# Kernel optimization log

Hardware: AMD Instinct MI355X
Metric: run time of the kernel (lower is better)

Reference implementation:

```python
import jax, jax.numpy as jnp
import numpy as np

N_NODES = 100000
N_EDGES = 1600000


def setup_inputs() -> dict:
    key = jax.random.key(0)
    ks = jax.random.split(key, 16)
    d_emb, d_mlp, d_lstm = 128, 256, 256
    B, C, T = 8, 4, 128
    return {
        "input_ids": jax.random.randint(ks[0], (B, C, T), 0, N_NODES, dtype=jnp.int64 if jax.config.jax_enable_x64 else jnp.int32),
        "input_mask": jnp.ones((B, C, T), dtype=jnp.int32),
        "labels": jax.random.uniform(ks[1], (B, C), dtype=jnp.float32),
        "src": jax.random.randint(ks[2], (N_EDGES,), 0, N_NODES),
        "dst": jax.random.randint(ks[3], (N_EDGES,), 0, N_NODES),
        "edge_value": jax.random.uniform(ks[4], (N_EDGES,), dtype=jnp.float32),
        "node_emb": jax.random.normal(ks[5], (N_NODES, d_emb), dtype=jnp.float32),
        "W1": jax.random.normal(ks[6], (d_mlp, d_emb), dtype=jnp.float32) * 0.05,
        "b1": jax.random.normal(ks[7], (d_mlp,), dtype=jnp.float32) * 0.05,
        "w_ih": jax.random.normal(ks[8], (4 * d_lstm, d_mlp), dtype=jnp.float32) * 0.05,
        "w_hh": jax.random.normal(ks[9], (4 * d_lstm, d_lstm), dtype=jnp.float32) * 0.05,
        "b_ih": jax.random.normal(ks[10], (4 * d_lstm,), dtype=jnp.float32) * 0.05,
        "b_hh": jax.random.normal(ks[11], (4 * d_lstm,), dtype=jnp.float32) * 0.05,
        "W2": jax.random.normal(ks[12], (1, d_lstm), dtype=jnp.float32) * 0.05,
        "b2": jax.random.normal(ks[13], (1,), dtype=jnp.float32) * 0.05,
    }


def reference(input_ids, input_mask, labels, src, dst, edge_value,
              node_emb, W1, b1, w_ih, w_hh, b_ih, b_hh, W2, b2):
    N = node_emb.shape[0]
    # edge-weighted mean message passing: u_mul_e('embedding','value') -> mean
    m = node_emb[src] * edge_value[:, None]                       # [E, d_emb]
    agg = jax.ops.segment_sum(m, dst, num_segments=N)             # [N, d_emb]
    cnt = jax.ops.segment_sum(jnp.ones_like(edge_value), dst, num_segments=N)
    h_nodes = agg / jnp.maximum(cnt, 1.0)[:, None]
    # linear1 on all nodes
    t_nodes = h_nodes @ W1.T + b1                                  # [N, d_mlp]
    B, C, T = input_ids.shape
    x = t_nodes[input_ids.reshape(B * C, T)]                       # [BC, T, d_mlp]
    lengths = input_mask.sum(axis=-1).reshape(B * C)               # [BC]
    H = w_hh.shape[1]

    def step(carry, xt):
        h, c = carry
        gates = xt @ w_ih.T + b_ih + h @ w_hh.T + b_hh
        i, f, g, o = jnp.split(gates, 4, axis=-1)  # torch LSTM gate order
        c = jax.nn.sigmoid(f) * c + jax.nn.sigmoid(i) * jnp.tanh(g)
        h = jax.nn.sigmoid(o) * jnp.tanh(c)
        return (h, c), h

    h0 = jnp.zeros((B * C, H), x.dtype)
    _, hs = jax.lax.scan(step, (h0, h0), jnp.swapaxes(x, 0, 1))    # [T, BC, H]
    hs = jnp.swapaxes(hs, 0, 1)                                    # [BC, T, H]
    idx = (lengths - 1).astype(jnp.int32)[:, None, None]
    h_last = jnp.take_along_axis(hs, jnp.broadcast_to(idx, (B * C, 1, H)), axis=1)[:, 0, :]
    scores = (h_last @ W2.T + b2).reshape(B, C)                    # [B, 4]
    p = jax.nn.softmax(scores, axis=1)
    # BCEWithLogits applied to softmaxed scores (as in the original)
    error = jnp.mean(jnp.maximum(p, 0) - p * labels + jnp.log1p(jnp.exp(-jnp.abs(p))))
    predictions = jnp.argmax(p, axis=1)
    return error, predictions
```

## Files before the change

### kernel.cpp

```cpp
#include <hip/hip_runtime.h>
#include <math.h>

#define NNODES 100000
#define NEDGES 1600000
#define NPOS   4096
#define NSEQ   32
#define TSTEPS 128

typedef float f32x4 __attribute__((ext_vector_type(4)));
typedef unsigned u32x4 __attribute__((ext_vector_type(4)));
typedef _Float16 h2v __attribute__((ext_vector_type(2)));

#define OFF_SLOT   0
#define OFF_AGG    400128
#define OFF_CNT    2497280
#define OFF_WF     2513664
#define OFF_BIASF  3037952
#define OFF_PREG   3042048
#define OFF_HS     19819264
#define OFF_WR  OFF_AGG
#define OFF_WL  (OFF_AGG + 98304)
#define OFF_WS  (OFF_AGG + 245760)

static __device__ __forceinline__ float fdot2(unsigned w, unsigned h, float acc) {
#if __has_builtin(__builtin_amdgcn_fdot2)
  h2v wv, hv;
  __builtin_memcpy(&wv, &w, 4);
  __builtin_memcpy(&hv, &h, 4);
  return __builtin_amdgcn_fdot2(wv, hv, acc, false);
#else
  asm("v_dot2_f32_f16 %0, %1, %2, %0" : "+v"(acc) : "v"(w), "v"(h));
  return acc;
#endif
}

static __device__ __forceinline__ float dotq(u32x4 w, u32x4 h, float a) {
  a = fdot2(w[0], h[0], a);
  a = fdot2(w[1], h[1], a);
  a = fdot2(w[2], h[2], a);
  a = fdot2(w[3], h[3], a);
  return a;
}

__global__ void k_init(int* slotmap, float* agg, float* cnt, float* hs0) {
  int i = blockIdx.x * blockDim.x + threadIdx.x;
  int stride = gridDim.x * blockDim.x;
  for (int idx = i; idx < 4096 * 128; idx += stride) agg[idx] = 0.f;
  for (int idx = i; idx < NNODES; idx += stride) slotmap[idx] = -1;
  for (int idx = i; idx < 4096; idx += stride) cnt[idx] = 0.f;
  for (int idx = i; idx < 8192; idx += stride) hs0[idx] = 0.f;
}

__global__ void k_mark(const int* __restrict__ input_ids, int* __restrict__ slotmap) {
  int p = blockIdx.x * blockDim.x + threadIdx.x;
  if (p < NPOS) atomicCAS(&slotmap[input_ids[p]], -1, p);
}

__global__ void k_edge(const int* __restrict__ src, const int* __restrict__ dst,
                       const float* __restrict__ ev, const float* __restrict__ emb,
                       const int* __restrict__ slotmap,
                       float* __restrict__ agg, float* __restrict__ cnt) {
  int e = blockIdx.x * 256 + threadIdx.x;
  int lane = threadIdx.x & 63;
  int d = dst[e];
  int slot = slotmap[d];
  int sn = 0; float vv = 0.f;
  if (slot >= 0) { sn = src[e]; vv = ev[e]; }
  unsigned long long m = __ballot(slot >= 0);
  while (m) {
    int j = __ffsll(m) - 1;
    m &= m - 1;
    int sl = __shfl(slot, j);
    int s2 = __shfl(sn, j);
    float v = __shfl(vv, j);
    float2 em = *(const float2*)&emb[(size_t)s2 * 128 + 2 * lane];
    atomicAdd(&agg[sl * 128 + 2 * lane],     em.x * v);
    atomicAdd(&agg[sl * 128 + 2 * lane + 1], em.y * v);
    if (lane == 0) atomicAdd(&cnt[sl], 1.f);
  }
}

__global__ void k_div(float* __restrict__ agg, const float* __restrict__ cnt) {
  int i = blockIdx.x * blockDim.x + threadIdx.x;
  agg[i] /= fmaxf(cnt[i >> 7], 1.f);
}

__global__ void k_fuse(const float* __restrict__ w_ih, const float* __restrict__ W1,
                       const float* __restrict__ b1, const float* __restrict__ b_ih,
                       const float* __restrict__ b_hh,
                       float* __restrict__ Wf, float* __restrict__ bf) {
  int row = blockIdx.x;
  int e = threadIdx.x;
  float acc = 0.f;
  for (int m2 = 0; m2 < 256; ++m2) acc += w_ih[row * 256 + m2] * W1[m2 * 128 + e];
  Wf[row * 128 + e] = acc;
  if (e == 0) {
    float bacc = b_ih[row] + b_hh[row];
    for (int m2 = 0; m2 < 256; ++m2) bacc += w_ih[row * 256 + m2] * b1[m2];
    bf[row] = bacc;
  }
}

__global__ __launch_bounds__(256, 2) void k_pregemm(
    const float* __restrict__ hnode, const float* __restrict__ Wf,
    const float* __restrict__ bf, const int* __restrict__ slotmap,
    const int* __restrict__ input_ids, float* __restrict__ preg) {
  __shared__ float Ash[64][132];
  __shared__ float Bsh[64][132];
  __shared__ int slots[64];
  int tid = threadIdx.x;
  int bm = (blockIdx.x & 63) * 64;
  int bn = (blockIdx.x >> 6) * 64;
  if (tid < 64) slots[tid] = slotmap[input_ids[bm + tid]];
  __syncthreads();
#pragma unroll
  for (int i = 0; i < 8; ++i) {
    int idx = tid + 256 * i;
    int r = idx >> 5, c = idx & 31;
    *(float4*)&Ash[r][c * 4] = *(const float4*)&hnode[slots[r] * 128 + c * 4];
    *(float4*)&Bsh[r][c * 4] = *(const float4*)&Wf[(bn + r) * 128 + c * 4];
  }
  __syncthreads();
  int tx = tid & 15, ty = tid >> 4;
  float acc[4][4] = {};
  for (int k = 0; k < 128; k += 4) {
    float4 a[4], bb[4];
#pragma unroll
    for (int i = 0; i < 4; ++i) a[i] = *(const float4*)&Ash[tx + 16 * i][k];
#pragma unroll
    for (int j = 0; j < 4; ++j) bb[j] = *(const float4*)&Bsh[ty + 16 * j][k];
#pragma unroll
    for (int i = 0; i < 4; ++i)
#pragma unroll
      for (int j = 0; j < 4; ++j)
        acc[i][j] += a[i].x * bb[j].x + a[i].y * bb[j].y + a[i].z * bb[j].z + a[i].w * bb[j].w;
  }
#pragma unroll
  for (int j = 0; j < 4; ++j) {
    int row = bn + ty + 16 * j;
    float bias = bf[row];
    int q  = row >> 8;
    int mm = (row >> 5) & 7;
    int dl = row & 31;
#pragma unroll
    for (int i = 0; i < 4; ++i) {
      int p = bm + tx + 16 * i;
      int s = p >> 7, tt = p & 127;
      preg[(((size_t)(tt * 32 + s) * 8 + mm) * 4 + q) * 32 + dl] = acc[i][j] + bias;
    }
  }
}

__global__ void k_wcvt(const float* __restrict__ w_hh, unsigned* __restrict__ wR,
                       unsigned* __restrict__ wL, unsigned* __restrict__ wS) {
  int idx = blockIdx.x * 256 + threadIdx.x;
  int row = idx >> 7;
  int j   = idx & 127;
  float x0 = w_hh[(size_t)row * 256 + 2 * j];
  float x1 = w_hh[(size_t)row * 256 + 2 * j + 1];
  union { _Float16 f[2]; unsigned u; } pk;
  pk.f[0] = (_Float16)x0;
  pk.f[1] = (_Float16)x1;
  int q = row >> 8, dd = row & 255;
  int kseg = j >> 5, p = j & 31;
  int c = p >> 2, l = p & 3;
  int tid = kseg * 256 + dd;
  if (q == 0 && c < 6) {
    wR[(c * 4 + l) * 1024 + tid] = pk.u;
  } else if (q == 0) {
    wL[((c - 6) * 1024 + tid) * 4 + l] = pk.u;
  } else if (q == 1 && c < 7) {
    wL[((2 + c) * 1024 + tid) * 4 + l] = pk.u;
  } else if (q == 1) {
    wS[(14 * 1024 + tid) * 4 + l] = pk.u;
  } else if (q == 2) {
    wS[(((c < 7) ? (2 * c) : 15) * 1024 + tid) * 4 + l] = pk.u;
  } else {
    wS[(((c < 7) ? (2 * c + 1) : 16) * 1024 + tid) * 4 + l] = pk.u;
  }
}

__global__ __launch_bounds__(1024) void k_lstm(
    const unsigned* __restrict__ wR, const unsigned* __restrict__ wL,
    const unsigned* __restrict__ wS, const float* __restrict__ preg,
    float* __restrict__ hs) {
  __shared__ __align__(16) unsigned whL[9 * 1024 * 4];
  __shared__ __align__(16) unsigned h16[128];
  __shared__ __align__(16) float    accb[3 * 256 * 4];
  const int tid  = threadIdx.x;
  const int s    = blockIdx.x;
  const int kseg = tid >> 8;
  const int d    = tid & 255;
  const bool owner = (kseg == 0);

  u32x4 rq[6];
#pragma unroll
  for (int qr = 0; qr < 6; ++qr)
#pragma unroll
    for (int l = 0; l < 4; ++l)
      rq[qr][l] = wR[(qr * 4 + l) * 1024 + tid];
  {
    const u32x4* src = (const u32x4*)wL;
    u32x4* dst = (u32x4*)whL;
#pragma unroll
    for (int lc = 0; lc < 9; ++lc)
      dst[lc * 1024 + tid] = src[lc * 1024 + tid];
  }
  if (tid < 128) h16[tid] = 0u;
  float c_st = 0.f;
  __syncthreads();

  const u32x4* hqp = (const u32x4*)h16 + kseg * 8;
  const u32x4* lq  = (const u32x4*)whL + tid;
  const u32x4* sq  = (const u32x4*)wS + tid;

  for (int t = 0; t < TSTEPS; ++t) {
    float pg[4] = {0.f, 0.f, 0.f, 0.f};
    if (owner) {
      const float* pb = preg + (((size_t)(t * 32 + s) * 8 + (d >> 5)) * 4) * 32
                        + (d & 31);
#pragma unroll
      for (int q = 0; q < 4; ++q) pg[q] = pb[q * 32];
    }
    float a0 = 0.f, a1 = 0.f, a2 = 0.f, a3 = 0.f;
#pragma unroll
    for (int c = 0; c < 8; ++c) {
      u32x4 h4 = hqp[c];
      u32x4 w0 = (c < 6) ? rq[c] : lq[(c - 6) * 1024];
      u32x4 w1 = (c < 7) ? lq[(2 + c) * 1024] : sq[14 * 1024];
      u32x4 w2 = sq[((c < 7) ? (2 * c) : 15) * 1024];
      u32x4 w3 = sq[((c < 7) ? (2 * c + 1) : 16) * 1024];
      a0 = dotq(w0, h4, a0);
      a1 = dotq(w1, h4, a1);
      a2 = dotq(w2, h4, a2);
      a3 = dotq(w3, h4, a3);
    }
    if (!owner) {
      f32x4 r; r.x = a0; r.y = a1; r.z = a2; r.w = a3;
      *(f32x4*)&accb[((kseg - 1) * 256 + d) * 4] = r;
    }
    __syncthreads();
    if (owner) {
      f32x4 r0 = *(const f32x4*)&accb[(0 * 256 + d) * 4];
      f32x4 r1 = *(const f32x4*)&accb[(1 * 256 + d) * 4];
      f32x4 r2 = *(const f32x4*)&accb[(2 * 256 + d) * 4];
      float gi = a0 + r0.x + r1.x + r2.x + pg[0];
      float gf = a1 + r0.y + r1.y + r2.y + pg[1];
      float gg = a2 + r0.z + r1.z + r2.z + pg[2];
      float go = a3 + r0.w + r1.w + r2.w + pg[3];
      float si = 1.f / (1.f + expf(-gi));
      float sf = 1.f / (1.f + expf(-gf));
      float so = 1.f / (1.f + expf(-go));
      float cc = sf * c_st + si * tanhf(gg);
      float hh = so * tanhf(cc);
      c_st = cc;
      ((_Float16*)h16)[d] = (_Float16)hh;
      hs[(size_t)(t + 1) * 8192 + s * 256 + d] = hh;
    }
    __syncthreads();
  }
}

__global__ void k_final(const float* __restrict__ hs, const int* __restrict__ mask,
                        const float* __restrict__ labels, const float* __restrict__ W2,
                        const float* __restrict__ b2, float* __restrict__ out) {
  __shared__ float scores[32];
  __shared__ float errpart[8];
  int tid = threadIdx.x;
  if (tid < 32) {
    int len = 0;
    for (int t = 0; t < 128; ++t) len += mask[tid * 128 + t];
    if (len < 1) len = 1;
    const float* hl = hs + (size_t)len * 8192 + tid * 256;
    float acc = b2[0];
    for (int k = 0; k < 256; ++k) acc += hl[k] * W2[k];
    scores[tid] = acc;
  }
  __syncthreads();
  if (tid < 8) {
    float sc[4];
#pragma unroll
    for (int i = 0; i < 4; ++i) sc[i] = scores[tid * 4 + i];
    float mx = fmaxf(fmaxf(sc[0], sc[1]), fmaxf(sc[2], sc[3]));
    float ex[4], ssum = 0.f;
#pragma unroll
    for (int i = 0; i < 4; ++i) { ex[i] = expf(sc[i] - mx); ssum += ex[i]; }
    float esum = 0.f; int am = 0; float best = -1e30f;
#pragma unroll
    for (int i = 0; i < 4; ++i) {
      float p = ex[i] / ssum;
      float li = labels[tid * 4 + i];
      esum += fmaxf(p, 0.f) - p * li + log1pf(expf(-fabsf(p)));
      if (p > best) { best = p; am = i; }
    }
    errpart[tid] = esum;
    out[1 + tid] = (float)am;
  }
  __syncthreads();
  if (tid == 0) {
    float e = 0.f;
    for (int i = 0; i < 8; ++i) e += errpart[i];
    out[0] = e / 32.f;
  }
}

extern "C" void kernel_launch(void* const* d_in, const int* in_sizes, int n_in,
                              void* d_out, int out_size, void* d_ws, size_t ws_size,
                              hipStream_t stream) {
  const int*   input_ids  = (const int*)d_in[0];
  const int*   input_mask = (const int*)d_in[1];
  const float* labels     = (const float*)d_in[2];
  const int*   src        = (const int*)d_in[3];
  const int*   dst        = (const int*)d_in[4];
  const float* ev         = (const float*)d_in[5];
  const float* node_emb   = (const float*)d_in[6];
  const float* W1         = (const float*)d_in[7];
  const float* b1         = (const float*)d_in[8];
  const float* w_ih       = (const float*)d_in[9];
  const float* w_hh       = (const float*)d_in[10];
  const float* b_ih       = (const float*)d_in[11];
  const float* b_hh       = (const float*)d_in[12];
  const float* W2         = (const float*)d_in[13];
  const float* b2         = (const float*)d_in[14];
  float* out = (float*)d_out;
  char* ws = (char*)d_ws;
  int*      slotmap = (int*)(ws + OFF_SLOT);
  float*    agg     = (float*)(ws + OFF_AGG);
  float*    cnt     = (float*)(ws + OFF_CNT);
  float*    Wf      = (float*)(ws + OFF_WF);
  float*    biasf   = (float*)(ws + OFF_BIASF);
  float*    preg    = (float*)(ws + OFF_PREG);
  float*    hs      = (float*)(ws + OFF_HS);
  unsigned* wRimg   = (unsigned*)(ws + OFF_WR);
  unsigned* wLimg   = (unsigned*)(ws + OFF_WL);
  unsigned* wSimg   = (unsigned*)(ws + OFF_WS);

  hipLaunchKernelGGL(k_init,    dim3(2048), dim3(256),  0, stream, slotmap, agg, cnt, hs);
  hipLaunchKernelGGL(k_mark,    dim3(16),   dim3(256),  0, stream, input_ids, slotmap);
  hipLaunchKernelGGL(k_edge,    dim3(6250), dim3(256),  0, stream, src, dst, ev, node_emb, slotmap, agg, cnt);
  hipLaunchKernelGGL(k_div,     dim3(2048), dim3(256),  0, stream, agg, cnt);
  hipLaunchKernelGGL(k_fuse,    dim3(1024), dim3(128),  0, stream, w_ih, W1, b1, b_ih, b_hh, Wf, biasf);
  hipLaunchKernelGGL(k_pregemm, dim3(1024), dim3(256),  0, stream, agg, Wf, biasf, slotmap, input_ids, preg);
  hipLaunchKernelGGL(k_wcvt,    dim3(512),  dim3(256),  0, stream, w_hh, wRimg, wLimg, wSimg);
  hipLaunchKernelGGL(k_lstm,    dim3(NSEQ), dim3(1024), 0, stream, wRimg, wLimg, wSimg, preg, hs);
  hipLaunchKernelGGL(k_final,   dim3(1),    dim3(64),   0, stream, hs, input_mask, labels, W2, b2, out);
}
```

Before: 334.0 us.

## Replace atomic edge scatter with counting-sort bucketing and per-slot accumulation

Edges whose destination is a referenced slot are counted, prefix-summed and bucketed into a compact per-slot edge list. One wave per slot then accumulates the weighted embeddings in registers and writes them once. This removes the float atomics on the aggregation buffer and the need to zero it. The cost is two extra passes over the edge arrays plus a single-block prefix-scan launch, and scatter order is nondeterministic, so float summation order can vary between runs.

```diff
diff --git a/kernel.cpp b/kernel.cpp
--- a/kernel.cpp
+++ b/kernel.cpp
@@ -42,12 +42,11 @@
   return a;
 }
 
-__global__ void k_init(int* slotmap, float* agg, float* cnt, float* hs0) {
+__global__ void k_init(int* slotmap, int* icnt, float* hs0) {
   int i = blockIdx.x * blockDim.x + threadIdx.x;
   int stride = gridDim.x * blockDim.x;
-  for (int idx = i; idx < 4096 * 128; idx += stride) agg[idx] = 0.f;
   for (int idx = i; idx < NNODES; idx += stride) slotmap[idx] = -1;
-  for (int idx = i; idx < 4096; idx += stride) cnt[idx] = 0.f;
+  for (int idx = i; idx < 4096; idx += stride) icnt[idx] = 0;
   for (int idx = i; idx < 8192; idx += stride) hs0[idx] = 0.f;
 }
 
@@ -56,33 +55,76 @@
   if (p < NPOS) atomicCAS(&slotmap[input_ids[p]], -1, p);
 }
 
-__global__ void k_edge(const int* __restrict__ src, const int* __restrict__ dst,
-                       const float* __restrict__ ev, const float* __restrict__ emb,
-                       const int* __restrict__ slotmap,
-                       float* __restrict__ agg, float* __restrict__ cnt) {
+__global__ void k_cnt(const int* __restrict__ dst, const int* __restrict__ slotmap,
+                      int* __restrict__ icnt) {
   int e = blockIdx.x * 256 + threadIdx.x;
+  int slot = slotmap[dst[e]];
+  if (slot >= 0) atomicAdd(&icnt[slot], 1);
+}
+
+__global__ void k_prefix(const int* __restrict__ icnt, int* __restrict__ offs,
+                         int* __restrict__ curs) {
+  __shared__ int part[256];
+  int tid = threadIdx.x;
+  int base = tid * 16;
+  int local[16];
+  int s = 0;
+  for (int i = 0; i < 16; ++i) { local[i] = s; s += icnt[base + i]; }
+  part[tid] = s;
+  __syncthreads();
+  for (int off = 1; off < 256; off <<= 1) {
+    int v = part[tid];
+    int add = (tid >= off) ? part[tid - off] : 0;
+    __syncthreads();
+    part[tid] = v + add;
+    __syncthreads();
+  }
+  int excl = (tid == 0) ? 0 : part[tid - 1];
+  for (int i = 0; i < 16; ++i) {
+    int o = excl + local[i];
+    offs[base + i] = o;
+    curs[base + i] = o;
+  }
+}
+
+__global__ void k_scat(const int* __restrict__ dst, const int* __restrict__ slotmap,
+                       const int* __restrict__ src, const float* __restrict__ ev,
+                       int* __restrict__ curs, int2* __restrict__ ebuf) {
+  int e = blockIdx.x * 256 + threadIdx.x;
+  int slot = slotmap[dst[e]];
+  if (slot >= 0) {
+    int idx = atomicAdd(&curs[slot], 1);
+    int2 r;
+    r.x = src[e];
+    r.y = __float_as_int(ev[e]);
+    ebuf[idx] = r;
+  }
+}
+
+__global__ void k_acc(const int2* __restrict__ ebuf, const int* __restrict__ offs,
+                      const int* __restrict__ icnt, const float* __restrict__ emb,
+                      float* __restrict__ agg) {
+  int wave = threadIdx.x >> 6;
   int lane = threadIdx.x & 63;
-  int d = dst[e];
-  int slot = slotmap[d];
-  int sn = 0; float vv = 0.f;
-  if (slot >= 0) { sn = src[e]; vv = ev[e]; }
-  unsigned long long m = __ballot(slot >= 0);
-  while (m) {
-    int j = __ffsll(m) - 1;
-    m &= m - 1;
-    int sl = __shfl(slot, j);
-    int s2 = __shfl(sn, j);
-    float v = __shfl(vv, j);
-    float2 em = *(const float2*)&emb[(size_t)s2 * 128 + 2 * lane];
-    atomicAdd(&agg[sl * 128 + 2 * lane],     em.x * v);
-    atomicAdd(&agg[sl * 128 + 2 * lane + 1], em.y * v);
-    if (lane == 0) atomicAdd(&cnt[sl], 1.f);
-  }
-}
-
-__global__ void k_div(float* __restrict__ agg, const float* __restrict__ cnt) {
+  int slot = blockIdx.x * 4 + wave;
+  int base = offs[slot], n = icnt[slot];
+  float a0 = 0.f, a1 = 0.f;
+  for (int i = 0; i < n; ++i) {
+    int2 r = ebuf[base + i];
+    float2 em = *(const float2*)&emb[(size_t)r.x * 128 + 2 * lane];
+    float v = __int_as_float(r.y);
+    a0 += em.x * v;
+    a1 += em.y * v;
+  }
+  float2 o;
+  o.x = a0;
+  o.y = a1;
+  *(float2*)&agg[slot * 128 + 2 * lane] = o;
+}
+
+__global__ void k_div(float* __restrict__ agg, const int* __restrict__ icnt) {
   int i = blockIdx.x * blockDim.x + threadIdx.x;
-  agg[i] /= fmaxf(cnt[i >> 7], 1.f);
+  agg[i] /= fmaxf((float)icnt[i >> 7], 1.f);
 }
 
 __global__ void k_fuse(const float* __restrict__ w_ih, const float* __restrict__ W1,
@@ -326,19 +368,25 @@
   char* ws = (char*)d_ws;
   int*      slotmap = (int*)(ws + OFF_SLOT);
   float*    agg     = (float*)(ws + OFF_AGG);
-  float*    cnt     = (float*)(ws + OFF_CNT);
+  int*      icnt    = (int*)(ws + OFF_CNT);
   float*    Wf      = (float*)(ws + OFF_WF);
+  int*      offs    = (int*)(ws + OFF_WF);
+  int*      curs    = (int*)(ws + OFF_WF + 16384);
   float*    biasf   = (float*)(ws + OFF_BIASF);
   float*    preg    = (float*)(ws + OFF_PREG);
+  int2*     ebuf    = (int2*)(ws + OFF_PREG);
   float*    hs      = (float*)(ws + OFF_HS);
   unsigned* wRimg   = (unsigned*)(ws + OFF_WR);
   unsigned* wLimg   = (unsigned*)(ws + OFF_WL);
   unsigned* wSimg   = (unsigned*)(ws + OFF_WS);
 
-  hipLaunchKernelGGL(k_init,    dim3(2048), dim3(256),  0, stream, slotmap, agg, cnt, hs);
+  hipLaunchKernelGGL(k_init,    dim3(512),  dim3(256),  0, stream, slotmap, icnt, hs);
   hipLaunchKernelGGL(k_mark,    dim3(16),   dim3(256),  0, stream, input_ids, slotmap);
-  hipLaunchKernelGGL(k_edge,    dim3(6250), dim3(256),  0, stream, src, dst, ev, node_emb, slotmap, agg, cnt);
-  hipLaunchKernelGGL(k_div,     dim3(2048), dim3(256),  0, stream, agg, cnt);
+  hipLaunchKernelGGL(k_cnt,     dim3(6250), dim3(256),  0, stream, dst, slotmap, icnt);
+  hipLaunchKernelGGL(k_prefix,  dim3(1),    dim3(256),  0, stream, icnt, offs, curs);
+  hipLaunchKernelGGL(k_scat,    dim3(6250), dim3(256),  0, stream, dst, slotmap, src, ev, curs, ebuf);
+  hipLaunchKernelGGL(k_acc,     dim3(1024), dim3(256),  0, stream, ebuf, offs, icnt, node_emb, agg);
+  hipLaunchKernelGGL(k_div,     dim3(2048), dim3(256),  0, stream, agg, icnt);
   hipLaunchKernelGGL(k_fuse,    dim3(1024), dim3(128),  0, stream, w_ih, W1, b1, b_ih, b_hh, Wf, biasf);
   hipLaunchKernelGGL(k_pregemm, dim3(1024), dim3(256),  0, stream, agg, Wf, biasf, slotmap, input_ids, preg);
   hipLaunchKernelGGL(k_wcvt,    dim3(512),  dim3(256),  0, stream, w_hh, wRimg, wLimg, wSimg);
```

Result: faster. 310.5 us (median of 2 runs) (-7.0%).
